# Kernel tuning notes

Hardware: AMD Instinct MI355X
Metric: run time of the kernel (lower is better)

## Reference

```python
import jax, jax.numpy as jnp
import numpy as np

N, E, B = 50000, 800000, 64
ND, ED, HID, NC = 64, 16, 128, 6
HEADS = [4, 4, 1]
CH = [32, 32, 128]
CONCAT = [True, True, False]

PNAMES = ['pW', 'pb'] + [f'{p}{l}' for l in range(3) for p in ['W', 'as', 'ad', 'ae', 'We', 'b', 'g', 'be']] + ['gW1', 'gb1', 'gW2', 'gb2', 'cW1', 'cb1', 'cW2', 'cb2']


def _gat_conv(x, src, dst, ea, W, a_s, a_d, a_e, We, b, heads, ch, concat):
    n = x.shape[0]
    xp = (x @ W).reshape(n, heads, ch)          # [N,H,C]
    al_src = (xp * a_s).sum(-1)                 # [N,H]
    al_dst = (xp * a_d).sum(-1)                 # [N,H]
    ep = (ea @ We).reshape(-1, heads, ch)       # [E,H,C]
    al_edge = (ep * a_e).sum(-1)                # [E,H]
    alpha = jax.nn.leaky_relu(al_src[src] + al_dst[dst] + al_edge, 0.2)
    # segment softmax over destination nodes
    amax = jax.ops.segment_max(alpha, dst, num_segments=n)
    ex = jnp.exp(alpha - amax[dst])
    den = jax.ops.segment_sum(ex, dst, num_segments=n)
    alpha = ex / (den[dst] + 1e-16)
    out = jax.ops.segment_sum(xp[src] * alpha[:, :, None], dst, num_segments=n)
    out = out.reshape(n, heads * ch) if concat else out.mean(axis=1)
    return out + b


def _layernorm(x, g, be):
    m = x.mean(-1, keepdims=True)
    v = ((x - m) ** 2).mean(-1, keepdims=True)
    return (x - m) / jnp.sqrt(v + 1e-5) * g + be


def _forward(x, edge_index, edge_attr, batch, params):
    src, dst = edge_index[0], edge_index[1]
    h = jax.nn.relu(x @ params['pW'] + params['pb'])
    for l in range(3):
        r = h
        h = _gat_conv(h, src, dst, edge_attr, params[f'W{l}'], params[f'as{l}'],
                      params[f'ad{l}'], params[f'ae{l}'], params[f'We{l}'], params[f'b{l}'],
                      HEADS[l], CH[l], CONCAT[l])
        h = _layernorm(h, params[f'g{l}'], params[f'be{l}'])
        h = jax.nn.elu(h)
        h = h + r
    # GlobalAttention pooling: gate MLP + segment softmax over graphs
    gate = jax.nn.relu(h @ params['gW1'] + params['gb1']) @ params['gW2'] + params['gb2']  # [N,1]
    gmax = jax.ops.segment_max(gate, batch, num_segments=B)
    ge = jnp.exp(gate - gmax[batch])
    gden = jax.ops.segment_sum(ge, batch, num_segments=B)
    att = ge / (gden[batch] + 1e-16)
    pooled = jax.ops.segment_sum(att * h, batch, num_segments=B)  # [B,HID]
    return jax.nn.relu(pooled @ params['cW1'] + params['cb1']) @ params['cW2'] + params['cb2']


def setup_inputs() -> dict:
    key = jax.random.key(0)
    ks = iter(jax.random.split(key, 64))
    nx = lambda: next(ks)
    rn = lambda shape, s=0.1: jax.random.normal(nx(), shape, jnp.float32) * s
    inp = {
        'x': jax.random.normal(nx(), (N, ND), jnp.float32),
        'edge_index': jax.random.randint(nx(), (2, E), 0, N),
        'edge_attr': jax.random.normal(nx(), (E, ED), jnp.float32),
        'batch': jnp.sort(jax.random.randint(nx(), (N,), 0, B)),
        'pW': rn((ND, HID)), 'pb': jnp.zeros((HID,), jnp.float32),
    }
    for l in range(3):
        h, c = HEADS[l], CH[l]
        inp[f'W{l}'] = rn((HID, h * c))
        inp[f'as{l}'] = rn((h, c))
        inp[f'ad{l}'] = rn((h, c))
        inp[f'ae{l}'] = rn((h, c))
        inp[f'We{l}'] = rn((ED, h * c))
        inp[f'b{l}'] = jnp.zeros((HID,), jnp.float32)
        inp[f'g{l}'] = jnp.ones((HID,), jnp.float32)
        inp[f'be{l}'] = jnp.zeros((HID,), jnp.float32)
    inp['gW1'] = rn((HID, HID // 2)); inp['gb1'] = jnp.zeros((HID // 2,), jnp.float32)
    inp['gW2'] = rn((HID // 2, 1)); inp['gb2'] = jnp.zeros((1,), jnp.float32)
    inp['cW1'] = rn((HID, HID // 2)); inp['cb1'] = jnp.zeros((HID // 2,), jnp.float32)
    inp['cW2'] = rn((HID // 2, NC)); inp['cb2'] = jnp.zeros((NC,), jnp.float32)
    return inp


def reference(x, edge_index, edge_attr, batch, pW, pb,
              W0, as0, ad0, ae0, We0, b0, g0, be0,
              W1, as1, ad1, ae1, We1, b1, g1, be1,
              W2, as2, ad2, ae2, We2, b2, g2, be2,
              gW1, gb1, gW2, gb2, cW1, cb1, cW2, cb2):
    params = dict(zip(PNAMES, (pW, pb, W0, as0, ad0, ae0, We0, b0, g0, be0,
                               W1, as1, ad1, ae1, We1, b1, g1, be1,
                               W2, as2, ad2, ae2, We2, b2, g2, be2,
                               gW1, gb1, gW2, gb2, cW1, cb1, cW2, cb2)))
    return _forward(x, edge_index, edge_attr, batch, params)
```

## Files before the change

### kernel.cpp

```cpp
#include <hip/hip_runtime.h>
#include <hip/hip_fp16.h>
#include <math.h>

#define N_NODES 50000
#define N_EDGES 800000
#define NB      64
#define ND      64
#define ED      16
#define HID     128
#define NC      6
#define POOL_SPLIT 32
#define SCAN_BLOCKS ((N_NODES + 255) / 256)
#define GEMM_BLOCKS ((N_NODES + 63) / 64)
#define DEG_BLOCKS  ((N_EDGES + 255) / 256)

typedef _Float16 f16;
typedef f16  half8  __attribute__((ext_vector_type(8)));
typedef float floatx4 __attribute__((ext_vector_type(4)));

__global__ void k_setup(const float* __restrict__ pW, const float* __restrict__ W0,
                        const float* __restrict__ W1, const float* __restrict__ W2,
                        const float* __restrict__ We0, const float* __restrict__ ae0,
                        const float* __restrict__ We1, const float* __restrict__ ae1,
                        const float* __restrict__ We2, const float* __restrict__ ae2,
                        int* __restrict__ deg, float* __restrict__ pooled,
                        float* __restrict__ WeAe,
                        f16* __restrict__ Wtp, f16* __restrict__ Wt0,
                        f16* __restrict__ Wt1, f16* __restrict__ Wt2) {
    int i = blockIdx.x * 256 + threadIdx.x;
    if (i < N_NODES) deg[i] = 0;
    if (i < NB * HID) pooled[i] = 0.f;
    if (i < 128 * 64) {
        int n = i / 64, k = i % 64;
        Wtp[i] = (f16)pW[k * 128 + n];
    }
    if (i < 128 * 128) {
        int n = i / 128, k = i % 128;
        Wt0[i] = (f16)W0[k * 128 + n];
        Wt1[i] = (f16)W1[k * 128 + n];
        Wt2[i] = (f16)W2[k * 128 + n];
    }
    if (i >= 60000 && i < 60144) {
        int t = i - 60000;
        if (t < 64) {
            int k = t >> 2, h = t & 3;
            float s = 0.f;
            for (int c = 0; c < 32; c++) s += We0[k * HID + h * 32 + c] * ae0[h * 32 + c];
            WeAe[k * 9 + h] = s;
        } else if (t < 128) {
            int tt = t - 64;
            int k = tt >> 2, h = tt & 3;
            float s = 0.f;
            for (int c = 0; c < 32; c++) s += We1[k * HID + h * 32 + c] * ae1[h * 32 + c];
            WeAe[k * 9 + 4 + h] = s;
        } else {
            int k = t - 128;
            float s = 0.f;
            for (int c = 0; c < HID; c++) s += We2[k * HID + c] * ae2[c];
            WeAe[k * 9 + 8] = s;
        }
    }
}

template <int K, int MODE, typename AT>
__device__ __forceinline__ void gemm_body(
        const AT* __restrict__ act, const f16* __restrict__ Wt,
        const float* __restrict__ bias, const float* __restrict__ as_,
        const float* __restrict__ ad_, __half* __restrict__ hout,
        __half* __restrict__ xp, float* __restrict__ al_src,
        float* __restrict__ al_dst, int blk) {
    constexpr int KP = K + 8;
    constexpr int OP = HID + 8;
    __shared__ __align__(16) f16 A[64 * OP];
    __shared__ float part_s[4][64];
    __shared__ float part_d[4][64];
    int tid = threadIdx.x;
    int base = blk * 64;

    if constexpr (sizeof(AT) == 4) {
        constexpr int NV = 64 * (K / 4) / 256;
        #pragma unroll
        for (int i = 0; i < NV; i++) {
            int v = tid + i * 256;
            int row = v / (K / 4), k4 = v % (K / 4);
            float4 xv = make_float4(0.f, 0.f, 0.f, 0.f);
            if (base + row < N_NODES)
                xv = *(const float4*)((const float*)act + (size_t)(base + row) * K + k4 * 4);
            f16* dp = &A[row * KP + k4 * 4];
            dp[0] = (f16)xv.x; dp[1] = (f16)xv.y; dp[2] = (f16)xv.z; dp[3] = (f16)xv.w;
        }
    } else {
        constexpr int NV = 64 * (K / 8) / 256;
        #pragma unroll
        for (int i = 0; i < NV; i++) {
            int v = tid + i * 256;
            int row = v / (K / 8), k8 = v % (K / 8);
            uint4 xv = make_uint4(0, 0, 0, 0);
            if (base + row < N_NODES)
                xv = *(const uint4*)((const __half*)act + (size_t)(base + row) * K + k8 * 8);
            *(uint4*)(&A[row * KP + k8 * 8]) = xv;
        }
    }
    __syncthreads();

    int w = tid >> 6, l = tid & 63;
    int lm = l & 15, q = l >> 4;
    floatx4 acc[4][2];
    #pragma unroll
    for (int mt = 0; mt < 4; mt++)
        #pragma unroll
        for (int j = 0; j < 2; j++)
            acc[mt][j] = (floatx4){0.f, 0.f, 0.f, 0.f};

    #pragma unroll
    for (int kt = 0; kt < K / 32; kt++) {
        int ko = kt * 32 + q * 8;
        half8 b0 = *(const half8*)(Wt + (size_t)(w * 32 + lm) * K + ko);
        half8 b1 = *(const half8*)(Wt + (size_t)(w * 32 + 16 + lm) * K + ko);
        #pragma unroll
        for (int mt = 0; mt < 4; mt++) {
            half8 a = *(const half8*)(&A[(mt * 16 + lm) * KP + ko]);
            acc[mt][0] = __builtin_amdgcn_mfma_f32_16x16x32_f16(a, b0, acc[mt][0], 0, 0, 0);
            acc[mt][1] = __builtin_amdgcn_mfma_f32_16x16x32_f16(a, b1, acc[mt][1], 0, 0, 0);
        }
    }

    if (MODE == 0) {
        float b0 = bias[w * 32 + lm];
        float b1 = bias[w * 32 + 16 + lm];
        __syncthreads();
        #pragma unroll
        for (int mt = 0; mt < 4; mt++)
            #pragma unroll
            for (int r = 0; r < 4; r++) {
                int row = mt * 16 + q * 4 + r;
                A[row * OP + w * 32 + lm]      = (f16)fmaxf(acc[mt][0][r] + b0, 0.f);
                A[row * OP + w * 32 + 16 + lm] = (f16)fmaxf(acc[mt][1][r] + b1, 0.f);
            }
        __syncthreads();
        #pragma unroll
        for (int i = 0; i < 4; i++) {
            int v = tid + i * 256;
            int row = v >> 4, c8 = v & 15;
            if (base + row < N_NODES) {
                float4 hv = *(const float4*)(&A[row * OP + c8 * 8]);
                *reinterpret_cast<float4*>(reinterpret_cast<char*>(hout) +
                    ((size_t)(base + row) * HID + c8 * 8) * 2) = hv;
            }
        }
    } else {
        float a0 = as_[w * 32 + lm], a1 = as_[w * 32 + 16 + lm];
        float e0 = ad_[w * 32 + lm], e1 = ad_[w * 32 + 16 + lm];
        float ps[4][4], pd[4][4];
        #pragma unroll
        for (int mt = 0; mt < 4; mt++)
            #pragma unroll
            for (int r = 0; r < 4; r++) {
                ps[mt][r] = acc[mt][0][r] * a0 + acc[mt][1][r] * a1;
                pd[mt][r] = acc[mt][0][r] * e0 + acc[mt][1][r] * e1;
            }
        #pragma unroll
        for (int off = 1; off < 16; off <<= 1)
            #pragma unroll
            for (int mt = 0; mt < 4; mt++)
                #pragma unroll
                for (int r = 0; r < 4; r++) {
                    ps[mt][r] += __shfl_xor(ps[mt][r], off, 64);
                    pd[mt][r] += __shfl_xor(pd[mt][r], off, 64);
                }
        if (MODE == 1) {
            if (lm == 0)
                #pragma unroll
                for (int mt = 0; mt < 4; mt++)
                    #pragma unroll
                    for (int r = 0; r < 4; r++) {
                        int n = base + mt * 16 + q * 4 + r;
                        if (n < N_NODES) {
                            al_src[n * 4 + w] = ps[mt][r];
                            al_dst[n * 4 + w] = pd[mt][r];
                        }
                    }
        } else {
            if (lm == 0)
                #pragma unroll
                for (int mt = 0; mt < 4; mt++)
                    #pragma unroll
                    for (int r = 0; r < 4; r++) {
                        part_s[w][mt * 16 + q * 4 + r] = ps[mt][r];
                        part_d[w][mt * 16 + q * 4 + r] = pd[mt][r];
                    }
        }
        __syncthreads();
        #pragma unroll
        for (int mt = 0; mt < 4; mt++)
            #pragma unroll
            for (int r = 0; r < 4; r++) {
                int row = mt * 16 + q * 4 + r;
                A[row * OP + w * 32 + lm]      = (f16)acc[mt][0][r];
                A[row * OP + w * 32 + 16 + lm] = (f16)acc[mt][1][r];
            }
        if (MODE == 2 && tid < 64) {
            int n = base + tid;
            if (n < N_NODES) {
                al_src[n] = part_s[0][tid] + part_s[1][tid] + part_s[2][tid] + part_s[3][tid];
                al_dst[n] = part_d[0][tid] + part_d[1][tid] + part_d[2][tid] + part_d[3][tid];
            }
        }
        __syncthreads();
        #pragma unroll
        for (int i = 0; i < 4; i++) {
            int v = tid + i * 256;
            int row = v >> 4, c8 = v & 15;
            if (base + row < N_NODES) {
                float4 hv = *(const float4*)(&A[row * OP + c8 * 8]);
                *reinterpret_cast<float4*>(reinterpret_cast<char*>(xp) +
                    ((size_t)(base + row) * HID + c8 * 8) * 2) = hv;
            }
        }
    }
}

__global__ __launch_bounds__(256) void k_proj_deg(
        const float* __restrict__ x, const f16* __restrict__ Wtp,
        const float* __restrict__ pb, __half* __restrict__ h,
        const int* __restrict__ dst, int* __restrict__ deg, int* __restrict__ rank) {
    if (blockIdx.x < GEMM_BLOCKS) {
        gemm_body<64, 0, float>(x, Wtp, pb, nullptr, nullptr, h, nullptr, nullptr, nullptr,
                                blockIdx.x);
    } else {
        int e = (blockIdx.x - GEMM_BLOCKS) * 256 + threadIdx.x;
        if (e < N_EDGES) rank[e] = atomicAdd(&deg[dst[e]], 1);
    }
}

template <int K, int MODE>
__global__ __launch_bounds__(256) void k_gemm(
        const __half* __restrict__ act, const f16* __restrict__ Wt,
        const float* __restrict__ as_, const float* __restrict__ ad_,
        __half* __restrict__ xp, float* __restrict__ al_src, float* __restrict__ al_dst) {
    gemm_body<K, MODE, __half>(act, Wt, nullptr, as_, ad_, nullptr, xp, al_src, al_dst,
                               blockIdx.x);
}

__global__ void k_scanA(const int* __restrict__ deg, int* __restrict__ bsum) {
    __shared__ int wsu[4];
    int t = threadIdx.x;
    int i = blockIdx.x * 256 + t;
    int d = (i < N_NODES) ? deg[i] : 0;
    int v = d;
    #pragma unroll
    for (int o = 32; o > 0; o >>= 1) v += __shfl_xor(v, o, 64);
    if ((t & 63) == 0) wsu[t >> 6] = v;
    __syncthreads();
    if (t == 0) bsum[blockIdx.x] = wsu[0] + wsu[1] + wsu[2] + wsu[3];
}

__global__ void k_scanC2(const int* __restrict__ deg, const int* __restrict__ bsum,
                         int* __restrict__ offs) {
    __shared__ int sc[256];
    __shared__ int wred[4];
    int t = threadIdx.x;
    int b = (t < (int)blockIdx.x) ? bsum[t] : 0;
    #pragma unroll
    for (int o = 32; o > 0; o >>= 1) b += __shfl_xor(b, o, 64);
    if ((t & 63) == 0) wred[t >> 6] = b;
    __syncthreads();
    int pre = wred[0] + wred[1] + wred[2] + wred[3];
    int i = blockIdx.x * 256 + t;
    int d = (i < N_NODES) ? deg[i] : 0;
    sc[t] = d;
    __syncthreads();
    for (int o = 1; o < 256; o <<= 1) {
        int v = (t >= o) ? sc[t - o] : 0;
        __syncthreads();
        sc[t] += v;
        __syncthreads();
    }
    if (i < N_NODES) offs[i] = pre + sc[t] - d;
    if (i == 0) offs[N_NODES] = N_EDGES;
}

__global__ void k_edge_build(const int* __restrict__ src, const int* __restrict__ dst,
                             const int* __restrict__ rank, const int* __restrict__ offs,
                             const float* __restrict__ ea, const float* __restrict__ WeAe,
                             float4* __restrict__ rec) {
    __shared__ float w[ED * 9];
    __shared__ float4 rs[256][4];
    __shared__ int rp[256];
    int tid = threadIdx.x;
    if (tid < ED * 9) w[tid] = WeAe[tid];
    __syncthreads();
    int e = blockIdx.x * 256 + tid;
    if (e < N_EDGES) {
        float ev[ED];
        const float4* ep4 = reinterpret_cast<const float4*>(ea + (size_t)e * ED);
        #pragma unroll
        for (int q = 0; q < 4; q++) {
            float4 v = ep4[q];
            ev[q * 4 + 0] = v.x; ev[q * 4 + 1] = v.y;
            ev[q * 4 + 2] = v.z; ev[q * 4 + 3] = v.w;
        }
        float r[9];
        #pragma unroll
        for (int j = 0; j < 9; j++) r[j] = 0.f;
        #pragma unroll
        for (int k = 0; k < ED; k++) {
            float evk = ev[k];
            #pragma unroll
            for (int j = 0; j < 9; j++) r[j] += evk * w[k * 9 + j];
        }
        int d = dst[e], s = src[e];
        rp[tid] = offs[d] + rank[e];
        rs[tid][0] = make_float4(r[0], r[1], r[2], r[3]);
        rs[tid][1] = make_float4(r[4], r[5], r[6], r[7]);
        rs[tid][2] = make_float4(r[8], __int_as_float(s), __int_as_float(d), 0.f);
        rs[tid][3] = make_float4(0.f, 0.f, 0.f, 0.f);
    } else {
        rp[tid] = -1;
    }
    __syncthreads();
    int g0 = tid >> 2, q = tid & 3;
    #pragma unroll
    for (int rr = 0; rr < 4; rr++) {
        int g = rr * 64 + g0;
        int p = rp[g];
        if (p >= 0) rec[(size_t)p * 4 + q] = rs[g][q];
    }
}

template <int H, int SLOT>
__global__ void k_node_agg(const int* __restrict__ offs, const float4* __restrict__ rec,
                           const float* __restrict__ al_src, const float* __restrict__ al_dst,
                           const __half* __restrict__ xp, const float* __restrict__ bias,
                           const float* __restrict__ g, const float* __restrict__ be,
                           const __half* __restrict__ hin, __half* __restrict__ hout) {
    int tid = threadIdx.x;
    int wave = tid >> 6;
    int lane = tid & 63;
    int n = blockIdx.x * 4 + wave;
    if (n >= N_NODES) return;
    int e0 = offs[n], e1 = offs[n + 1];
    int side = lane >> 4;
    int cl = lane & 15;
    int c = cl * 8;
    int h = cl >> 2;
    float ald = (H == 4) ? al_dst[n * 4 + h] : al_dst[n];
    float acc[8] = {0.f, 0.f, 0.f, 0.f, 0.f, 0.f, 0.f, 0.f};
    float den = 0.f;

    auto fetchw = [&](int i, int& s, float& wv) {
        if (i < e1) {
            const float* rb = (const float*)(rec + (size_t)i * 4);
            s = __float_as_int(rb[9]);
            float r = (H == 4) ? rb[SLOT * 4 + h] : rb[8];
            float al = ((H == 4) ? al_src[s * 4 + h] : al_src[s]) + ald + r;
            al = (al >= 0.f) ? al : 0.2f * al;
            wv = __expf(al);
        } else { s = 0; wv = 0.f; }
    };
    auto accum = [&](uint4 r, float wv) {
        union { uint4 u; __half2 h2[4]; } t2; t2.u = r;
        #pragma unroll
        for (int j = 0; j < 4; j++) {
            float2 f = __half22float2(t2.h2[j]);
            acc[j * 2]     += wv * f.x;
            acc[j * 2 + 1] += wv * f.y;
        }
        den += wv;
    };

    int i = e0 + side;
    int sA, sB, sC, sD; float wA, wB, wC, wD;
    fetchw(i, sA, wA);
    fetchw(i + 4, sB, wB);
    fetchw(i + 8, sC, wC);
    fetchw(i + 12, sD, wD);
    while (i < e1) {
        uint4 rA = *reinterpret_cast<const uint4*>(xp + (size_t)sA * HID + c);
        uint4 rB = *reinterpret_cast<const uint4*>(xp + (size_t)sB * HID + c);
        uint4 rC = *reinterpret_cast<const uint4*>(xp + (size_t)sC * HID + c);
        uint4 rD = *reinterpret_cast<const uint4*>(xp + (size_t)sD * HID + c);
        int tA, tB, tC, tD; float vA, vB, vC, vD;
        fetchw(i + 16, tA, vA);
        fetchw(i + 20, tB, vB);
        fetchw(i + 24, tC, vC);
        fetchw(i + 28, tD, vD);
        accum(rA, wA);
        accum(rB, wB);
        accum(rC, wC);
        accum(rD, wD);
        sA = tA; wA = vA; sB = tB; wB = vB;
        sC = tC; wC = vC; sD = tD; wD = vD;
        i += 16;
    }
    #pragma unroll
    for (int j = 0; j < 8; j++) {
        acc[j] += __shfl_xor(acc[j], 16, 64);
        acc[j] += __shfl_xor(acc[j], 32, 64);
    }
    den += __shfl_xor(den, 16, 64);
    den += __shfl_xor(den, 32, 64);

    float inv = 1.f / (den + 1e-16f);
    float v[8];
    const float4 bv0 = *reinterpret_cast<const float4*>(bias + c);
    const float4 bv1 = *reinterpret_cast<const float4*>(bias + c + 4);
    v[0] = acc[0] * inv + bv0.x; v[1] = acc[1] * inv + bv0.y;
    v[2] = acc[2] * inv + bv0.z; v[3] = acc[3] * inv + bv0.w;
    v[4] = acc[4] * inv + bv1.x; v[5] = acc[5] * inv + bv1.y;
    v[6] = acc[6] * inv + bv1.z; v[7] = acc[7] * inv + bv1.w;
    float s8 = v[0] + v[1] + v[2] + v[3] + v[4] + v[5] + v[6] + v[7];
    #pragma unroll
    for (int o = 8; o > 0; o >>= 1) s8 += __shfl_xor(s8, o, 64);
    float mean = s8 * (1.f / HID);
    float q8 = 0.f;
    float d[8];
    #pragma unroll
    for (int j = 0; j < 8; j++) { d[j] = v[j] - mean; q8 += d[j] * d[j]; }
    #pragma unroll
    for (int o = 8; o > 0; o >>= 1) q8 += __shfl_xor(q8, o, 64);
    float rstd = rsqrtf(q8 * (1.f / HID) + 1e-5f);
    if (side < 2) {
        int co = c + side * 4;
        int j0 = side * 4;
        const float4 gv  = *reinterpret_cast<const float4*>(g + co);
        const float4 bev = *reinterpret_cast<const float4*>(be + co);
        float y0 = d[j0]     * rstd * gv.x + bev.x;
        float y1 = d[j0 + 1] * rstd * gv.y + bev.y;
        float y2 = d[j0 + 2] * rstd * gv.z + bev.z;
        float y3 = d[j0 + 3] * rstd * gv.w + bev.w;
        y0 = (y0 > 0.f) ? y0 : (__expf(y0) - 1.f);
        y1 = (y1 > 0.f) ? y1 : (__expf(y1) - 1.f);
        y2 = (y2 > 0.f) ? y2 : (__expf(y2) - 1.f);
        y3 = (y3 > 0.f) ? y3 : (__expf(y3) - 1.f);
        uint2 ru = *reinterpret_cast<const uint2*>(hin + (size_t)n * HID + co);
        union { uint2 u; __half2 h2[2]; } tr; tr.u = ru;
        float2 r01 = __half22float2(tr.h2[0]);
        float2 r23 = __half22float2(tr.h2[1]);
        union { uint2 u; __half2 h2[2]; } to;
        to.h2[0] = __floats2half2_rn(y0 + r01.x, y1 + r01.y);
        to.h2[1] = __floats2half2_rn(y2 + r23.x, y3 + r23.y);
        *reinterpret_cast<uint2*>(hout + (size_t)n * HID + co) = to.u;
    }
}

__global__ void k_gate(const __half* __restrict__ h, const float* __restrict__ gW1,
                       const float* __restrict__ gb1, const float* __restrict__ gW2,
                       const float* __restrict__ gb2, const int* __restrict__ batch,
                       float* __restrict__ gate, int* __restrict__ goff) {
    __shared__ float hs[16][HID];
    int tid = threadIdx.x;
    int base = blockIdx.x * 16;
    if (tid < 16) {
        int n = base + tid;
        int cur = batch[n];
        int prev = (n == 0) ? -1 : batch[n - 1];
        for (int gg = prev + 1; gg <= cur; gg++) goff[gg] = n;
        if (n == N_NODES - 1)
            for (int gg = cur + 1; gg <= NB; gg++) goff[gg] = N_NODES;
    }
    {
        int nn = tid >> 4, k8 = tid & 15;
        uint4 hv = *reinterpret_cast<const uint4*>(h + (size_t)(base + nn) * HID + k8 * 8);
        union { uint4 u; __half2 h2[4]; } th; th.u = hv;
        #pragma unroll
        for (int j = 0; j < 4; j++) {
            float2 f = __half22float2(th.h2[j]);
            hs[nn][k8 * 8 + j * 2]     = f.x;
            hs[nn][k8 * 8 + j * 2 + 1] = f.y;
        }
    }
    __syncthreads();
    int c = tid & 63;
    int wave = tid >> 6;
    float acc[4] = {0.f, 0.f, 0.f, 0.f};
    #pragma unroll 8
    for (int k = 0; k < HID; k++) {
        float wv = gW1[k * 64 + c];
        #pragma unroll
        for (int q = 0; q < 4; q++) acc[q] += hs[wave * 4 + q][k] * wv;
    }
    float b1 = gb1[c], w2 = gW2[c];
    float p[4];
    #pragma unroll
    for (int q = 0; q < 4; q++) p[q] = fmaxf(acc[q] + b1, 0.f) * w2;
    #pragma unroll
    for (int o = 32; o > 0; o >>= 1) {
        #pragma unroll
        for (int q = 0; q < 4; q++) p[q] += __shfl_xor(p[q], o, 64);
    }
    if (c == 0) {
        float b2 = gb2[0];
        #pragma unroll
        for (int q = 0; q < 4; q++) gate[base + wave * 4 + q] = p[q] + b2;
    }
}

__global__ void k_gmaxden(const float* __restrict__ gate, const int* __restrict__ goff,
                          float* __restrict__ gmax, float* __restrict__ gden) {
    int b = blockIdx.x;
    int t = threadIdx.x;
    __shared__ float red[256];
    int s = goff[b], e = goff[b + 1];
    float m = -__builtin_inff();
    for (int n = s + t; n < e; n += 256) m = fmaxf(m, gate[n]);
    red[t] = m;
    __syncthreads();
    for (int o = 128; o > 0; o >>= 1) { if (t < o) red[t] = fmaxf(red[t], red[t + o]); __syncthreads(); }
    m = red[0];
    __syncthreads();
    float d = 0.f;
    for (int n = s + t; n < e; n += 256) d += __expf(gate[n] - m);
    red[t] = d;
    __syncthreads();
    for (int o = 128; o > 0; o >>= 1) { if (t < o) red[t] += red[t + o]; __syncthreads(); }
    if (t == 0) { gmax[b] = m; gden[b] = red[0]; }
}

__global__ void k_pool(const __half* __restrict__ h, const float* __restrict__ gate,
                       const float* __restrict__ gmax, const float* __restrict__ gden,
                       const int* __restrict__ goff, float* __restrict__ pooled) {
    int b = blockIdx.x;
    int part = blockIdx.y;
    int c = threadIdx.x;
    int s = goff[b], e = goff[b + 1];
    float m = gmax[b];
    float dinv = 1.f / (gden[b] + 1e-16f);
    float acc = 0.f;
    for (int n = s + part; n < e; n += POOL_SPLIT) {
        float att = __expf(gate[n] - m) * dinv;
        acc += att * __half2float(h[(size_t)n * HID + c]);
    }
    atomicAdd(&pooled[b * HID + c], acc);
}

__global__ void k_head(const float* __restrict__ pooled, const float* __restrict__ cW1,
                       const float* __restrict__ cb1, const float* __restrict__ cW2,
                       const float* __restrict__ cb2, float* __restrict__ out) {
    int b = blockIdx.x;
    int t = threadIdx.x;
    __shared__ float pr[HID];
    __shared__ float tr[64];
    pr[t] = pooled[b * HID + t];
    pr[t + 64] = pooled[b * HID + t + 64];
    __syncthreads();
    float a = cb1[t];
    #pragma unroll 8
    for (int k = 0; k < HID; k++) a += pr[k] * cW1[k * 64 + t];
    tr[t] = fmaxf(a, 0.f);
    __syncthreads();
    if (t < NC) {
        float o = cb2[t];
        #pragma unroll
        for (int k = 0; k < 64; k++) o += tr[k] * cW2[k * NC + t];
        out[b * NC + t] = o;
    }
}

extern "C" void kernel_launch(void* const* d_in, const int* in_sizes, int n_in,
                              void* d_out, int out_size, void* d_ws, size_t ws_size,
                              hipStream_t stream) {
    (void)in_sizes; (void)n_in; (void)out_size; (void)ws_size;
    const float* x     = (const float*)d_in[0];
    const int*   ei    = (const int*)d_in[1];
    const float* ea    = (const float*)d_in[2];
    const int*   batch = (const int*)d_in[3];
    const float* pW    = (const float*)d_in[4];
    const float* pb    = (const float*)d_in[5];
    const float *W[3], *as_[3], *ad_[3], *ae_[3], *We[3], *bb[3], *gg[3], *be[3];
    for (int l = 0; l < 3; l++) {
        int base = 6 + 8 * l;
        W[l]   = (const float*)d_in[base + 0];
        as_[l] = (const float*)d_in[base + 1];
        ad_[l] = (const float*)d_in[base + 2];
        ae_[l] = (const float*)d_in[base + 3];
        We[l]  = (const float*)d_in[base + 4];
        bb[l]  = (const float*)d_in[base + 5];
        gg[l]  = (const float*)d_in[base + 6];
        be[l]  = (const float*)d_in[base + 7];
    }
    const float* gW1 = (const float*)d_in[30];
    const float* gb1 = (const float*)d_in[31];
    const float* gW2 = (const float*)d_in[32];
    const float* gb2 = (const float*)d_in[33];
    const float* cW1 = (const float*)d_in[34];
    const float* cb1 = (const float*)d_in[35];
    const float* cW2 = (const float*)d_in[36];
    const float* cb2 = (const float*)d_in[37];
    float* out = (float*)d_out;

    char* p = (char*)d_ws;
    auto take = [&](size_t bytes) -> char* {
        char* r = p;
        p += (bytes + 255) & ~(size_t)255;
        return r;
    };
    __half* h0      = (__half*)take((size_t)N_NODES * HID * 2);
    __half* h1      = (__half*)take((size_t)N_NODES * HID * 2);
    __half* xp      = (__half*)take((size_t)N_NODES * HID * 2);
    float*  al_src  = (float*)take((size_t)N_NODES * 4 * 4);
    float*  al_dst  = (float*)take((size_t)N_NODES * 4 * 4);
    float4* rec     = (float4*)take((size_t)N_EDGES * 64);
    int*    deg     = (int*)take((size_t)N_NODES * 4);
    int*    offs    = (int*)take((size_t)(N_NODES + 1) * 4);
    int*    rank    = (int*)take((size_t)N_EDGES * 4);
    int*    bsum    = (int*)take(256 * 4);
    float*  WeAe    = (float*)take(ED * 9 * 4);
    float*  gate    = (float*)take((size_t)N_NODES * 4);
    float*  gmax    = (float*)take(NB * 4);
    float*  gden    = (float*)take(NB * 4);
    int*    goff    = (int*)take((NB + 1) * 4);
    float*  pooled  = (float*)take(NB * HID * 4);
    f16*    Wtp     = (f16*)take(128 * 64 * 2);
    f16*    Wt0     = (f16*)take(128 * 128 * 2);
    f16*    Wt1     = (f16*)take(128 * 128 * 2);
    f16*    Wt2     = (f16*)take(128 * 128 * 2);
    f16*    Wt[3]   = {Wt0, Wt1, Wt2};

    const int* src = ei;
    const int* dst = ei + N_EDGES;

    k_setup<<<256, 256, 0, stream>>>(pW, W[0], W[1], W[2], We[0], ae_[0], We[1], ae_[1],
                                     We[2], ae_[2], deg, pooled, WeAe, Wtp, Wt0, Wt1, Wt2);
    k_proj_deg<<<GEMM_BLOCKS + DEG_BLOCKS, 256, 0, stream>>>(x, Wtp, pb, h0, dst, deg, rank);
    k_scanA<<<SCAN_BLOCKS, 256, 0, stream>>>(deg, bsum);
    k_scanC2<<<SCAN_BLOCKS, 256, 0, stream>>>(deg, bsum, offs);
    k_edge_build<<<DEG_BLOCKS, 256, 0, stream>>>(src, dst, rank, offs, ea, WeAe, rec);

    __half* hc = h0;
    __half* hn = h1;
    k_gemm<128, 1><<<GEMM_BLOCKS, 256, 0, stream>>>(hc, Wt[0], as_[0], ad_[0], xp, al_src, al_dst);
    k_node_agg<4, 0><<<(N_NODES + 3) / 4, 256, 0, stream>>>(offs, rec, al_src, al_dst, xp,
                                                            bb[0], gg[0], be[0], hc, hn);
    { __half* t = hc; hc = hn; hn = t; }
    k_gemm<128, 1><<<GEMM_BLOCKS, 256, 0, stream>>>(hc, Wt[1], as_[1], ad_[1], xp, al_src, al_dst);
    k_node_agg<4, 1><<<(N_NODES + 3) / 4, 256, 0, stream>>>(offs, rec, al_src, al_dst, xp,
                                                            bb[1], gg[1], be[1], hc, hn);
    { __half* t = hc; hc = hn; hn = t; }
    k_gemm<128, 2><<<GEMM_BLOCKS, 256, 0, stream>>>(hc, Wt[2], as_[2], ad_[2], xp, al_src, al_dst);
    k_node_agg<1, 0><<<(N_NODES + 3) / 4, 256, 0, stream>>>(offs, rec, al_src, al_dst, xp,
                                                            bb[2], gg[2], be[2], hc, hn);
    { __half* t = hc; hc = hn; hn = t; }

    k_gate<<<N_NODES / 16, 256, 0, stream>>>(hc, gW1, gb1, gW2, gb2, batch, gate, goff);
    k_gmaxden<<<NB, 256, 0, stream>>>(gate, goff, gmax, gden);
    k_pool<<<dim3(NB, POOL_SPLIT), HID, 0, stream>>>(hc, gate, gmax, gden, goff, pooled);
    k_head<<<NB, 64, 0, stream>>>(pooled, cW1, cb1, cW2, cb2, out);
}
```

Baseline: 484.0 us.

## Compute edge attention weights once per edge-head and share via LDS

Previously each of the 16 lanes covering a node's channels recomputed the edge logit, exp and source index redundantly for every edge. Now each wave computes each edge-head weight exactly once (one lane per edge-head) in chunks of 16 or 64 edges. The weights and source indices go through shared memory before the gather-accumulate loop. This cuts redundant loads and exp work, but drops the software prefetch pipelining. It also relies on intra-wave LDS visibility without a barrier, and short-degree nodes waste lanes per chunk.

```diff
diff --git a/kernel.cpp b/kernel.cpp
--- a/kernel.cpp
+++ b/kernel.cpp
@@ -334,6 +334,8 @@
                            const __half* __restrict__ xp, const float* __restrict__ bias,
                            const float* __restrict__ g, const float* __restrict__ be,
                            const __half* __restrict__ hin, __half* __restrict__ hout) {
+    __shared__ float ws[4][64];
+    __shared__ int   ss[4][64];
     int tid = threadIdx.x;
     int wave = tid >> 6;
     int lane = tid & 63;
@@ -344,20 +346,14 @@
     int cl = lane & 15;
     int c = cl * 8;
     int h = cl >> 2;
-    float ald = (H == 4) ? al_dst[n * 4 + h] : al_dst[n];
+    int pa_h   = (H == 4) ? (lane & 3) : 0;
+    int pa_off = (H == 4) ? (lane >> 2) : lane;
+    float pa_ald = (H == 4) ? al_dst[n * 4 + pa_h] : al_dst[n];
+    const int CHUNK = (H == 4) ? 16 : 64;
+
     float acc[8] = {0.f, 0.f, 0.f, 0.f, 0.f, 0.f, 0.f, 0.f};
     float den = 0.f;
 
-    auto fetchw = [&](int i, int& s, float& wv) {
-        if (i < e1) {
-            const float* rb = (const float*)(rec + (size_t)i * 4);
-            s = __float_as_int(rb[9]);
-            float r = (H == 4) ? rb[SLOT * 4 + h] : rb[8];
-            float al = ((H == 4) ? al_src[s * 4 + h] : al_src[s]) + ald + r;
-            al = (al >= 0.f) ? al : 0.2f * al;
-            wv = __expf(al);
-        } else { s = 0; wv = 0.f; }
-    };
     auto accum = [&](uint4 r, float wv) {
         union { uint4 u; __half2 h2[4]; } t2; t2.u = r;
         #pragma unroll
@@ -369,30 +365,48 @@
         den += wv;
     };
 
-    int i = e0 + side;
-    int sA, sB, sC, sD; float wA, wB, wC, wD;
-    fetchw(i, sA, wA);
-    fetchw(i + 4, sB, wB);
-    fetchw(i + 8, sC, wC);
-    fetchw(i + 12, sD, wD);
-    while (i < e1) {
-        uint4 rA = *reinterpret_cast<const uint4*>(xp + (size_t)sA * HID + c);
-        uint4 rB = *reinterpret_cast<const uint4*>(xp + (size_t)sB * HID + c);
-        uint4 rC = *reinterpret_cast<const uint4*>(xp + (size_t)sC * HID + c);
-        uint4 rD = *reinterpret_cast<const uint4*>(xp + (size_t)sD * HID + c);
-        int tA, tB, tC, tD; float vA, vB, vC, vD;
-        fetchw(i + 16, tA, vA);
-        fetchw(i + 20, tB, vB);
-        fetchw(i + 24, tC, vC);
-        fetchw(i + 28, tD, vD);
-        accum(rA, wA);
-        accum(rB, wB);
-        accum(rC, wC);
-        accum(rD, wD);
-        sA = tA; wA = vA; sB = tB; wB = vB;
-        sC = tC; wC = vC; sD = tD; wD = vD;
-        i += 16;
-    }
+    for (int cb = e0; cb < e1; cb += CHUNK) {
+        int i = cb + pa_off;
+        float wv = 0.f;
+        int s = 0;
+        if (i < e1) {
+            const float* rb = (const float*)(rec + (size_t)i * 4);
+            s = __float_as_int(rb[9]);
+            float r = (H == 4) ? rb[SLOT * 4 + pa_h] : rb[8];
+            float al = ((H == 4) ? al_src[s * 4 + pa_h] : al_src[s]) + pa_ald + r;
+            al = (al >= 0.f) ? al : 0.2f * al;
+            wv = __expf(al);
+        }
+        ws[wave][lane] = wv;
+        if (H == 4) {
+            if (pa_h == 0) ss[wave][pa_off] = s;
+        } else {
+            ss[wave][lane] = s;
+        }
+        if (H == 4) {
+            #pragma unroll
+            for (int k = 0; k < 4; k++) {
+                int eloc = side + 4 * k;
+                int sg = ss[wave][eloc];
+                float wk = ws[wave][eloc * 4 + h];
+                uint4 r = *reinterpret_cast<const uint4*>(xp + (size_t)sg * HID + c);
+                accum(r, wk);
+            }
+        } else {
+            #pragma unroll
+            for (int kk = 0; kk < 4; kk++) {
+                #pragma unroll
+                for (int k = 0; k < 4; k++) {
+                    int eloc = side + 4 * (kk * 4 + k);
+                    int sg = ss[wave][eloc];
+                    float wk = ws[wave][eloc];
+                    uint4 r = *reinterpret_cast<const uint4*>(xp + (size_t)sg * HID + c);
+                    accum(r, wk);
+                }
+            }
+        }
+    }
+
     #pragma unroll
     for (int j = 0; j < 8; j++) {
         acc[j] += __shfl_xor(acc[j], 16, 64);
```

Result: no change. 479.5 us (-0.9%).
